# Kernel optimization log

Hardware: AMD Instinct MI355X
Metric: run time of the kernel (lower is better)

The kernel has to match this reference:

```python
import jax, jax.numpy as jnp
import numpy as np

B, Hm, Wm, Dm = 1, 32, 32, 32
N = Hm * Wm * Dm
C = 128
HEADS, DH = 8, 16
G = 32
L = 2
OUT = 1


def _ln(x, g, b):
    mu = jnp.mean(x, -1, keepdims=True)
    var = jnp.mean((x - mu) ** 2, -1, keepdims=True)
    return (x - mu) * jax.lax.rsqrt(var + 1e-5) * g + b


def setup_inputs() -> dict:
    key = jax.random.key(0)
    ks = iter(jax.random.split(key, 64))
    def nrm(shape, s=0.02):
        return jax.random.normal(next(ks), shape, jnp.float32) * s
    return {
        "x": jax.random.normal(next(ks), (B, N, 3), jnp.float32),
        "fx": jax.random.normal(next(ks), (B, N, 1), jnp.float32),
        "pre_w1": nrm((4, 2 * C)), "pre_b1": jnp.zeros((2 * C,), jnp.float32),
        "pre_w2": nrm((2 * C, C)), "pre_b2": jnp.zeros((C,), jnp.float32),
        "placeholder": jax.random.uniform(next(ks), (C,), jnp.float32) / C,
        "ln1_g": jnp.ones((L, C), jnp.float32), "ln1_b": jnp.zeros((L, C), jnp.float32),
        "convx_w": nrm((L, C, C, 3, 3, 3)), "convx_b": jnp.zeros((L, C), jnp.float32),
        "convfx_w": nrm((L, C, C, 3, 3, 3)), "convfx_b": jnp.zeros((L, C), jnp.float32),
        "slice_w": nrm((L, DH, G), 0.1), "slice_b": jnp.zeros((L, G), jnp.float32),
        "temperature": jnp.full((L, 1, HEADS, 1, 1), 0.5, jnp.float32),
        "wq": nrm((L, DH, DH), 0.1), "wk": nrm((L, DH, DH), 0.1), "wv": nrm((L, DH, DH), 0.1),
        "wo": nrm((L, HEADS * DH, C)), "bo": jnp.zeros((L, C), jnp.float32),
        "ln2_g": jnp.ones((L, C), jnp.float32), "ln2_b": jnp.zeros((L, C), jnp.float32),
        "mlp_w1": nrm((L, C, C)), "mlp_b1": jnp.zeros((L, C), jnp.float32),
        "mlp_w2": nrm((L, C, C)), "mlp_b2": jnp.zeros((L, C), jnp.float32),
        "ln3_g": jnp.ones((C,), jnp.float32), "ln3_b": jnp.zeros((C,), jnp.float32),
        "out_w": nrm((C, OUT)), "out_b": jnp.zeros((OUT,), jnp.float32),
    }


def _conv3d(x, w, b):
    # x: [B,C,H,W,D], w: [O,I,3,3,3], SAME padding (kernel//2) as torch Conv3d
    y = jax.lax.conv_general_dilated(x, w, (1, 1, 1), "SAME",
                                     dimension_numbers=("NCDHW", "OIDHW", "NCDHW"))
    return y + b[None, :, None, None, None]


def _physics_attn(z, cw_x, cb_x, cw_fx, cb_fx, sw, sb, temp, wq, wk, wv, wo, bo):
    # z: [B, N, C] -> structured mesh conv projections -> slice attention
    xg = z.reshape(B, Hm, Wm, Dm, C).transpose(0, 4, 1, 2, 3)  # [B,C,H,W,D]

    def split_heads(t):  # [B,I,H,W,D] -> [B,heads,N,dh]
        return t.transpose(0, 2, 3, 4, 1).reshape(B, N, HEADS, DH).transpose(0, 2, 1, 3)

    x_mid = split_heads(_conv3d(xg, cw_x, cb_x))
    fx_mid = split_heads(_conv3d(xg, cw_fx, cb_fx))
    # slice assignment weights: [B,heads,N,G], temperature-scaled softmax
    slice_logits = (x_mid @ sw + sb) / temp
    swt = jax.nn.softmax(slice_logits, axis=-1)
    norm = jnp.sum(swt, axis=2)  # [B,heads,G]
    tok = jnp.einsum("bhnc,bhng->bhgc", fx_mid, swt) / (norm + 1e-5)[..., None]
    q, k, v = tok @ wq, tok @ wk, tok @ wv  # [B,heads,G,dh]
    attn = jax.nn.softmax((q @ k.transpose(0, 1, 3, 2)) * (DH ** -0.5), axis=-1)
    ot = attn @ v  # [B,heads,G,dh]
    out = jnp.einsum("bhgc,bhng->bhnc", ot, swt)  # de-slice back to tokens
    out = out.transpose(0, 2, 1, 3).reshape(B, N, HEADS * DH)
    return out @ wo + bo


def reference(x, fx, pre_w1, pre_b1, pre_w2, pre_b2, placeholder,
              ln1_g, ln1_b, convx_w, convx_b, convfx_w, convfx_b,
              slice_w, slice_b, temperature, wq, wk, wv, wo, bo,
              ln2_g, ln2_b, mlp_w1, mlp_b1, mlp_w2, mlp_b2,
              ln3_g, ln3_b, out_w, out_b):
    h = jnp.concatenate([x, fx], axis=-1)  # [B,N,space+fun]
    z = jax.nn.gelu(h @ pre_w1 + pre_b1, approximate=False) @ pre_w2 + pre_b2 + placeholder
    for l in range(L):
        zn = _ln(z, ln1_g[l], ln1_b[l])
        z = _physics_attn(zn, convx_w[l], convx_b[l], convfx_w[l], convfx_b[l],
                          slice_w[l], slice_b[l], temperature[l],
                          wq[l], wk[l], wv[l], wo[l], bo[l]) + z
        zn = _ln(z, ln2_g[l], ln2_b[l])
        z = jax.nn.gelu(zn @ mlp_w1[l] + mlp_b1[l], approximate=False) @ mlp_w2[l] + mlp_b2[l] + z
    return _ln(z, ln3_g, ln3_b) @ out_w + out_b
```

## Files before the change

kernel.cpp:

```cpp
#include <hip/hip_runtime.h>
#include <hip/hip_bf16.h>

#define DEV __device__ __forceinline__

constexpr int N   = 32768;
constexpr int TOTAL_IN = 2038481;

constexpr int OFF_X        = 0;
constexpr int OFF_FX       = 98304;
constexpr int OFF_PRE_W1   = 131072;
constexpr int OFF_PRE_B1   = 132096;
constexpr int OFF_PRE_W2   = 132352;
constexpr int OFF_PRE_B2   = 165120;
constexpr int OFF_PLACE    = 165248;
constexpr int OFF_LN1_G    = 165376;
constexpr int OFF_LN1_B    = 165632;
constexpr int OFF_CONVX_W  = 165888;
constexpr int OFF_CONVX_B  = 1050624;
constexpr int OFF_CONVFX_W = 1050880;
constexpr int OFF_CONVFX_B = 1935616;
constexpr int OFF_SLICE_W  = 1935872;
constexpr int OFF_SLICE_B  = 1936896;
constexpr int OFF_TEMP     = 1936960;
constexpr int OFF_WQ       = 1936976;
constexpr int OFF_WK       = 1937488;
constexpr int OFF_WV       = 1938000;
constexpr int OFF_WO       = 1938512;
constexpr int OFF_BO       = 1971280;
constexpr int OFF_LN2_G    = 1971536;
constexpr int OFF_LN2_B    = 1971792;
constexpr int OFF_MLP_W1   = 1972048;
constexpr int OFF_MLP_B1   = 2004816;
constexpr int OFF_MLP_W2   = 2005072;
constexpr int OFF_MLP_B2   = 2037840;
constexpr int OFF_LN3_G    = 2038096;
constexpr int OFF_LN3_B    = 2038224;
constexpr int OFF_OUT_W    = 2038352;
constexpr int OFF_OUT_B    = 2038480;

__device__ __constant__ int d_PRE[32] = {
  0, 98304, 131072, 132096, 132352, 165120, 165248, 165376, 165632,
  165888, 1050624, 1050880, 1935616, 1935872, 1936896, 1936960, 1936976,
  1937488, 1938000, 1938512, 1971280, 1971536, 1971792, 1972048, 2004816,
  2005072, 2037840, 2038096, 2038224, 2038352, 2038480, 2038481
};

constexpr size_t F_IN   = 16;
constexpr size_t F_WT   = 2038512;
constexpr size_t F_Z    = F_WT   + 1769472;
constexpr size_t F_ZN   = F_Z    + 4194304;
constexpr size_t F_CONV = F_ZN   + 4194304;
constexpr size_t F_SWT  = F_CONV + 8388608;
constexpr size_t F_TOKP = F_SWT  + 8388608;
constexpr size_t F_TOK2 = F_TOKP + 1114112;
constexpr size_t F_OT   = F_TOK2 + 34816;
constexpr size_t F_WP   = F_OT   + 4096;
constexpr size_t F_END  = F_WP   + 65536;

struct InPtrs { const void* p[31]; };

typedef short short8v  __attribute__((ext_vector_type(8)));
typedef float float4v  __attribute__((ext_vector_type(4)));
#define MFMA16(A,B,C) __builtin_amdgcn_mfma_f32_16x16x32_bf16(A,B,C,0,0,0)

DEV float geluf(float x) { return 0.5f * x * (1.0f + erff(x * 0.70710678118654752f)); }
DEV short f2bs(float x) { union { __hip_bfloat16 h; short s; } c; c.h = __float2bfloat16(x); return c.s; }

__global__ void k_convert(InPtrs ptrs, float* __restrict__ ws) {
  const unsigned tw = *(const unsigned*)ptrs.p[15];
  const bool isbf = (tw == 0x3F003F00u);
  int stride = gridDim.x * blockDim.x;
  for (int e = blockIdx.x * blockDim.x + threadIdx.x; e < TOTAL_IN; e += stride) {
    int lo = 0, hi = 30;
#pragma unroll
    for (int it = 0; it < 5; ++it) {
      int mid = (lo + hi + 1) >> 1;
      if (e >= d_PRE[mid]) lo = mid; else hi = mid - 1;
    }
    int loc = e - d_PRE[lo];
    float v;
    if (isbf) {
      unsigned short u = ((const unsigned short*)ptrs.p[lo])[loc];
      unsigned uu = ((unsigned)u) << 16;
      v = __uint_as_float(uu);
    } else {
      v = ((const float*)ptrs.p[lo])[loc];
    }
    ws[F_IN + e] = v;
  }
}

__global__ void k_wtrans(const float* __restrict__ ip, short* __restrict__ wtf) {
  int f = blockIdx.x * 256 + threadIdx.x;
  if (f >= 221184) return;
  int lane = f & 63;
  int rest = f >> 6;
  int ntile = rest & 15;
  int r2 = rest >> 4;
  int layer = r2 / 108;
  int kt = r2 - layer * 108;
  int icb = kt / 27, tap = kt - icb * 27;
  int oc = ntile * 16 + (lane & 15);
  int ic0 = icb * 32 + (lane >> 4) * 8;
  const float* cw = ip + (oc < 128 ? OFF_CONVX_W : OFF_CONVFX_W);
  int o = oc & 127;
  const float* src = cw + ((size_t)(layer * 128 + o) * 128) * 27 + tap;
  short8v out;
#pragma unroll
  for (int j = 0; j < 8; ++j) out[j] = f2bs(src[(ic0 + j) * 27]);
  *(short8v*)(wtf + (size_t)f * 8) = out;
}

__global__ void k_wpack(const float* __restrict__ ip, short* __restrict__ wp) {
  int f = blockIdx.x * 256 + threadIdx.x;
  if (f >= 16384) return;
  int lane = f & 63;
  int t = f >> 6;
  int srcoff, kt, nt;
  if (t < 64) { srcoff = OFF_PRE_W2; kt = t >> 3; nt = t & 7; }
  else {
    int r = t - 64, l = r / 96, r2 = r - l * 96;
    int which = r2 >> 5, idx2 = r2 & 31;
    kt = idx2 >> 3; nt = idx2 & 7;
    srcoff = (which == 0 ? OFF_MLP_W1 : (which == 1 ? OFF_MLP_W2 : OFF_WO)) + l * 16384;
  }
  int k0 = kt * 32 + (lane >> 4) * 8;
  int n = nt * 16 + (lane & 15);
  const float* src = ip + srcoff + (size_t)k0 * 128 + n;
  short8v out;
#pragma unroll
  for (int j = 0; j < 8; ++j) out[j] = f2bs(src[(size_t)j * 128]);
  *(short8v*)(wp + (size_t)f * 8) = out;
}

__global__ __launch_bounds__(256)
void k_prenet(const float* __restrict__ ip, const short* __restrict__ wp,
              float* __restrict__ z, short* __restrict__ znb) {
  __shared__ float w1s[1024], b1s[256], cvec[128], g1s[128], be1s[128];
  __shared__ float xv[64][4];
  __shared__ __align__(16) short ts[64 * 264];
  int tid = threadIdx.x;
  int wv = tid >> 6, lane = tid & 63;
  int m = lane & 15, q = lane >> 4;
  int n0 = blockIdx.x * 64;
  for (int i = tid; i < 1024; i += 256) w1s[i] = ip[OFF_PRE_W1 + i];
  b1s[tid] = ip[OFF_PRE_B1 + tid];
  if (tid < 128) {
    cvec[tid] = ip[OFF_PRE_B2 + tid] + ip[OFF_PLACE + tid];
    g1s[tid]  = ip[OFF_LN1_G + tid];
    be1s[tid] = ip[OFF_LN1_B + tid];
  }
  if (tid < 64) {
    xv[tid][0] = ip[OFF_X + (n0 + tid) * 3 + 0];
    xv[tid][1] = ip[OFF_X + (n0 + tid) * 3 + 1];
    xv[tid][2] = ip[OFF_X + (n0 + tid) * 3 + 2];
    xv[tid][3] = ip[OFF_FX + n0 + tid];
  }
  __syncthreads();
  {
    float w0 = w1s[tid], wA = w1s[256 + tid], wB = w1s[512 + tid], wC = w1s[768 + tid];
    float bb = b1s[tid];
    for (int t = 0; t < 64; ++t) {
      float hv = bb + xv[t][0] * w0 + xv[t][1] * wA + xv[t][2] * wB + xv[t][3] * wC;
      ts[t * 264 + tid] = f2bs(geluf(hv));
    }
  }
  __syncthreads();
  const short8v* pwf = (const short8v*)wp;
  float4v acc[8];
#pragma unroll
  for (int nt = 0; nt < 8; ++nt) acc[nt] = (float4v){0.f, 0.f, 0.f, 0.f};
  for (int kt = 0; kt < 8; ++kt) {
    short8v A = *(const short8v*)(ts + (wv * 16 + m) * 264 + kt * 32 + q * 8);
#pragma unroll
    for (int nt = 0; nt < 8; ++nt)
      acc[nt] = MFMA16(A, pwf[(kt * 8 + nt) * 64 + lane], acc[nt]);
  }
  float vz[8][4];
#pragma unroll
  for (int nt = 0; nt < 8; ++nt) {
    int col = nt * 16 + m;
#pragma unroll
    for (int r = 0; r < 4; ++r) {
      vz[nt][r] = acc[nt][r] + cvec[col];
      z[(size_t)(n0 + wv * 16 + q * 4 + r) * 128 + col] = vz[nt][r];
    }
  }
#pragma unroll
  for (int r = 0; r < 4; ++r) {
    float s1 = 0.f, s2 = 0.f;
#pragma unroll
    for (int nt = 0; nt < 8; ++nt) { float v = vz[nt][r]; s1 += v; s2 += v * v; }
#pragma unroll
    for (int off = 1; off < 16; off <<= 1) { s1 += __shfl_xor(s1, off); s2 += __shfl_xor(s2, off); }
    float mu = s1 * (1.0f / 128.0f);
    float var = s2 * (1.0f / 128.0f) - mu * mu;
    float rst = 1.0f / sqrtf(var + 1e-5f);
    size_t rowb = (size_t)(n0 + wv * 16 + q * 4 + r) * 128;
#pragma unroll
    for (int nt = 0; nt < 8; ++nt) {
      int col = nt * 16 + m;
      znb[rowb + col] = f2bs((vz[nt][r] - mu) * rst * g1s[col] + be1s[col]);
    }
  }
}

__global__ __launch_bounds__(256)
void k_conv(const float* __restrict__ ip, const short* __restrict__ znb,
            const short* __restrict__ wtf, float* __restrict__ cv, int layer) {
  __shared__ __align__(16) short halo[13056];
  int tid = threadIdx.x;
  int wv = tid >> 6, lane = tid & 63;
  int m = lane & 15, q = lane >> 4;
  int n0 = blockIdx.x * 64;
  int h = n0 >> 10, w0 = (n0 >> 5) & 31;
  float bias_r[4];
#pragma unroll
  for (int nt = 0; nt < 4; ++nt) {
    int oc = (wv * 4 + nt) * 16 + m;
    bias_r[nt] = (oc < 128) ? ip[OFF_CONVX_B + layer * 128 + oc]
                            : ip[OFF_CONVFX_B + layer * 128 + (oc - 128)];
  }
  float4v acc[4][4];
#pragma unroll
  for (int a = 0; a < 4; ++a)
#pragma unroll
    for (int b = 0; b < 4; ++b) acc[a][b] = (float4v){0.f, 0.f, 0.f, 0.f};

  const short8v* wf = (const short8v*)wtf + (size_t)layer * 110592 + (wv * 4) * 64 + lane;
  short8v bc0 = wf[0], bc1 = wf[64], bc2 = wf[128], bc3 = wf[192];

  int tap = 0, icb = 0;
  for (int kt = 0; kt < 108; ++kt) {
    if (tap == 0) {
      __syncthreads();
      for (int pr = tid; pr < 408; pr += 256) {
        int line = pr / 34, dpos = pr - line * 34;
        int hh2 = h + (line >> 2) - 1, ww2 = w0 + (line & 3) - 1, dd2 = dpos - 1;
        bool ok = ((unsigned)hh2 < 32u) && ((unsigned)ww2 < 32u) && ((unsigned)dd2 < 32u);
        int tok = (hh2 << 10) + (ww2 << 5) + dd2;
#pragma unroll
        for (int qq = 0; qq < 4; ++qq) {
          short8v v = (short8v){0, 0, 0, 0, 0, 0, 0, 0};
          if (ok) v = *(const short8v*)(znb + (size_t)tok * 128 + icb * 32 + qq * 8);
          *(short8v*)(halo + qq * 3264 + pr * 8) = v;
        }
      }
      __syncthreads();
    }
    int ktn = (kt + 1 < 108) ? kt + 1 : kt;
    const short8v* wn = wf + (size_t)ktn * 1024;
    short8v bn0 = wn[0], bn1 = wn[64], bn2 = wn[128], bn3 = wn[192];

    int ta = tap / 9, rem = tap - ta * 9, tb = rem / 3, tc = rem - tb * 3;
    const short* hp = halo + q * 3264 + (((ta * 4 + tb) * 34) + tc + m) * 8;
    short8v A0 = *(const short8v*)(hp);
    short8v A1 = *(const short8v*)(hp + 128);
    short8v A2 = *(const short8v*)(hp + 272);
    short8v A3 = *(const short8v*)(hp + 400);

    acc[0][0] = MFMA16(A0, bc0, acc[0][0]);
    acc[1][0] = MFMA16(A1, bc0, acc[1][0]);
    acc[2][0] = MFMA16(A2, bc0, acc[2][0]);
    acc[3][0] = MFMA16(A3, bc0, acc[3][0]);
    acc[0][1] = MFMA16(A0, bc1, acc[0][1]);
    acc[1][1] = MFMA16(A1, bc1, acc[1][1]);
    acc[2][1] = MFMA16(A2, bc1, acc[2][1]);
    acc[3][1] = MFMA16(A3, bc1, acc[3][1]);
    acc[0][2] = MFMA16(A0, bc2, acc[0][2]);
    acc[1][2] = MFMA16(A1, bc2, acc[1][2]);
    acc[2][2] = MFMA16(A2, bc2, acc[2][2]);
    acc[3][2] = MFMA16(A3, bc2, acc[3][2]);
    acc[0][3] = MFMA16(A0, bc3, acc[0][3]);
    acc[1][3] = MFMA16(A1, bc3, acc[1][3]);
    acc[2][3] = MFMA16(A2, bc3, acc[2][3]);
    acc[3][3] = MFMA16(A3, bc3, acc[3][3]);

    bc0 = bn0; bc1 = bn1; bc2 = bn2; bc3 = bn3;
    if (++tap == 27) { tap = 0; ++icb; }
  }
#pragma unroll
  for (int mt = 0; mt < 4; ++mt) {
    float* cp = cv + (size_t)(n0 + mt * 16 + q * 4) * 256 + (wv * 4) * 16 + m;
#pragma unroll
    for (int nt = 0; nt < 4; ++nt) {
#pragma unroll
      for (int r = 0; r < 4; ++r)
        cp[(size_t)r * 256 + nt * 16] = acc[mt][nt][r] + bias_r[nt];
    }
  }
}

__global__ __launch_bounds__(256)
void k_slice(const float* __restrict__ ip, const float* __restrict__ cv,
             short* __restrict__ swtb, float* __restrict__ tokp, int layer) {
  __shared__ float sws[512], sbs[32], its[8];
  __shared__ float swl[32 * 257];
  __shared__ float fxl[32 * 128];
  int tid = threadIdx.x;
  for (int i = tid; i < 512; i += 256) sws[i] = ip[OFF_SLICE_W + layer * 512 + i];
  if (tid < 32) sbs[tid] = ip[OFF_SLICE_B + layer * 32 + tid];
  if (tid < 8)  its[tid] = 1.0f / ip[OFF_TEMP + layer * 8 + tid];
  float4 ta0 = make_float4(0,0,0,0), ta1 = ta0, ta2 = ta0, ta3 = ta0;
  float np = 0.f;
  for (int s = 0; s < 4; ++s) {
    int tbase = blockIdx.x * 128 + s * 32;
    __syncthreads();
    for (int i = tid; i < 1024; i += 256) {
      int t = i >> 5, c4 = (i & 31) * 4;
      *(float4*)&fxl[t * 128 + c4] = *(const float4*)&cv[(size_t)(tbase + t) * 256 + 128 + c4];
    }
    {
      int t = tid >> 3, hh = tid & 7;
      float xm[16];
#pragma unroll
      for (int qq = 0; qq < 4; ++qq)
        *(float4*)&xm[qq * 4] = *(const float4*)&cv[(size_t)(tbase + t) * 256 + hh * 16 + qq * 4];
      float lg[32];
      float itv = its[hh];
#pragma unroll
      for (int g = 0; g < 32; ++g) {
        float sacc = sbs[g];
#pragma unroll
        for (int j = 0; j < 16; ++j) sacc += xm[j] * sws[j * 32 + g];
        lg[g] = sacc * itv;
      }
      float mx = -1e30f;
#pragma unroll
      for (int g = 0; g < 32; ++g) mx = fmaxf(mx, lg[g]);
      float sum = 0.f;
#pragma unroll
      for (int g = 0; g < 32; ++g) { lg[g] = expf(lg[g] - mx); sum += lg[g]; }
      float inv = 1.0f / sum;
#pragma unroll
      for (int g = 0; g < 32; ++g) {
        lg[g] *= inv;
        swl[t * 257 + hh * 32 + g] = lg[g];
      }
#pragma unroll
      for (int qq = 0; qq < 4; ++qq) {
        short8v pk;
#pragma unroll
        for (int j = 0; j < 8; ++j) pk[j] = f2bs(lg[qq * 8 + j]);
        *(short8v*)(swtb + (size_t)(tbase + t) * 256 + hh * 32 + qq * 8) = pk;
      }
    }
    __syncthreads();
    {
      int ah = tid >> 5, ag = tid & 31;
      for (int t2 = 0; t2 < 32; ++t2) {
        float sv = swl[t2 * 257 + ah * 32 + ag];
        np += sv;
        const float* f = &fxl[t2 * 128 + ah * 16];
        float4 f0 = *(const float4*)&f[0], f1 = *(const float4*)&f[4];
        float4 f2 = *(const float4*)&f[8], f3 = *(const float4*)&f[12];
        ta0.x += sv * f0.x; ta0.y += sv * f0.y; ta0.z += sv * f0.z; ta0.w += sv * f0.w;
        ta1.x += sv * f1.x; ta1.y += sv * f1.y; ta1.z += sv * f1.z; ta1.w += sv * f1.w;
        ta2.x += sv * f2.x; ta2.y += sv * f2.y; ta2.z += sv * f2.z; ta2.w += sv * f2.w;
        ta3.x += sv * f3.x; ta3.y += sv * f3.y; ta3.z += sv * f3.z; ta3.w += sv * f3.w;
      }
    }
  }
  int ah = tid >> 5, ag = tid & 31;
  size_t base = (size_t)blockIdx.x * 4352 + (size_t)(ah * 32 + ag) * 16;
  *(float4*)&tokp[base + 0]  = ta0;
  *(float4*)&tokp[base + 4]  = ta1;
  *(float4*)&tokp[base + 8]  = ta2;
  *(float4*)&tokp[base + 12] = ta3;
  tokp[(size_t)blockIdx.x * 4352 + 4096 + ah * 32 + ag] = np;
}

__global__ void k_tokred1(const float* __restrict__ tokp, float* __restrict__ tok2) {
  int ogrp = blockIdx.x % 17, bgrp = blockIdx.x / 17;
  int o = ogrp * 256 + threadIdx.x;
  float s = 0.f;
  int b0 = bgrp * 32;
#pragma unroll 8
  for (int b = b0; b < b0 + 32; ++b) s += tokp[(size_t)b * 4352 + o];
  tok2[(size_t)bgrp * 4352 + o] = s;
}

__global__ __launch_bounds__(256)
void k_attn(const float* __restrict__ ip, const float* __restrict__ tok2,
            float* __restrict__ ot, int layer) {
  __shared__ float trs[4352];
  __shared__ float kk[256 * 17], vv[256 * 17];
  int tid = threadIdx.x;
  for (int i = tid; i < 4352; i += 256) {
    float s = 0.f;
#pragma unroll
    for (int b = 0; b < 8; ++b) s += tok2[(size_t)b * 4352 + i];
    trs[i] = s;
  }
  __syncthreads();
  int hh = tid >> 5;
  const float* wq = ip + OFF_WQ + layer * 256;
  const float* wk = ip + OFF_WK + layer * 256;
  const float* wv = ip + OFF_WV + layer * 256;
  float inv = 1.0f / (trs[4096 + tid] + 1e-5f);
  float t[16];
#pragma unroll
  for (int c = 0; c < 16; ++c) t[c] = trs[tid * 16 + c] * inv;
  float q[16];
#pragma unroll
  for (int c = 0; c < 16; ++c) {
    float aq = 0.f, ak = 0.f, av = 0.f;
#pragma unroll
    for (int j = 0; j < 16; ++j) {
      float tv = t[j];
      aq += tv * wq[j * 16 + c];
      ak += tv * wk[j * 16 + c];
      av += tv * wv[j * 16 + c];
    }
    q[c] = aq;
    kk[tid * 17 + c] = ak;
    vv[tid * 17 + c] = av;
  }
  __syncthreads();
  float sc[32];
  float mx = -1e30f;
#pragma unroll
  for (int g2 = 0; g2 < 32; ++g2) {
    float s = 0.f;
#pragma unroll
    for (int c = 0; c < 16; ++c) s += q[c] * kk[(hh * 32 + g2) * 17 + c];
    s *= 0.25f;
    sc[g2] = s; mx = fmaxf(mx, s);
  }
  float sum = 0.f;
#pragma unroll
  for (int g2 = 0; g2 < 32; ++g2) { sc[g2] = expf(sc[g2] - mx); sum += sc[g2]; }
  float inv2 = 1.0f / sum;
  float o[16];
#pragma unroll
  for (int c = 0; c < 16; ++c) o[c] = 0.f;
#pragma unroll
  for (int g2 = 0; g2 < 32; ++g2) {
    float p = sc[g2] * inv2;
#pragma unroll
    for (int c = 0; c < 16; ++c) o[c] += p * vv[(hh * 32 + g2) * 17 + c];
  }
#pragma unroll
  for (int c = 0; c < 16; ++c) ot[tid * 16 + c] = o[c];
}

__global__ __launch_bounds__(256)
void k_fused(const float* __restrict__ ip, const short* __restrict__ swtb,
             const float* __restrict__ ot, const short* __restrict__ wp,
             float* __restrict__ z, short* __restrict__ znb,
             void* __restrict__ dout, const void* __restrict__ tempraw, int layer) {
  __shared__ __align__(16) short otb[4096];
  __shared__ __align__(16) short al[8704];
  __shared__ __align__(16) short znt[8704];
  __shared__ float bol[128], b1s[128], b2s[128], g2s[128], be2s[128], lng[128], lnb[128], ows[128];
  int tid = threadIdx.x;
  int wv = tid >> 6, lane = tid & 63;
  int m = lane & 15, q = lane >> 4;
  int n0 = blockIdx.x * 64;
  if (tid < 128) {
    bol[tid]  = ip[OFF_BO + layer * 128 + tid];
    b1s[tid]  = ip[OFF_MLP_B1 + layer * 128 + tid];
    b2s[tid]  = ip[OFF_MLP_B2 + layer * 128 + tid];
    g2s[tid]  = ip[OFF_LN2_G + layer * 128 + tid];
    be2s[tid] = ip[OFF_LN2_B + layer * 128 + tid];
    if (layer == 0) {
      lng[tid] = ip[OFF_LN1_G + 128 + tid];
      lnb[tid] = ip[OFF_LN1_B + 128 + tid];
      ows[tid] = 0.f;
    } else {
      lng[tid] = ip[OFF_LN3_G + tid];
      lnb[tid] = ip[OFF_LN3_B + tid];
      ows[tid] = ip[OFF_OUT_W + tid];
    }
  }
  for (int i = tid; i < 4096; i += 256) {
    int h = i >> 9, r = i & 511, ln = r >> 3, j = r & 7;
    int g = (ln >> 4) * 8 + j, dh = ln & 15;
    otb[i] = f2bs(ot[h * 512 + g * 16 + dh]);
  }
  __syncthreads();
  float4v accd[8];
#pragma unroll
  for (int h = 0; h < 8; ++h) accd[h] = (float4v){0.f, 0.f, 0.f, 0.f};
#pragma unroll
  for (int h = 0; h < 8; ++h) {
    short8v A = *(const short8v*)(swtb + (size_t)(n0 + wv * 16 + m) * 256 + h * 32 + q * 8);
    accd[h] = MFMA16(A, *(const short8v*)(otb + h * 512 + lane * 8), accd[h]);
  }
#pragma unroll
  for (int h = 0; h < 8; ++h)
#pragma unroll
    for (int r = 0; r < 4; ++r)
      al[(wv * 16 + q * 4 + r) * 136 + h * 16 + m] = f2bs(accd[h][r]);
  __syncthreads();
  const short8v* wof = (const short8v*)(wp + (size_t)(128 + 96 * layer) * 512);
  float4v a2[8];
#pragma unroll
  for (int nt = 0; nt < 8; ++nt) a2[nt] = (float4v){0.f, 0.f, 0.f, 0.f};
  for (int kt = 0; kt < 4; ++kt) {
    short8v A = *(const short8v*)(al + (wv * 16 + m) * 136 + kt * 32 + q * 8);
#pragma unroll
    for (int nt = 0; nt < 8; ++nt)
      a2[nt] = MFMA16(A, wof[(kt * 8 + nt) * 64 + lane], a2[nt]);
  }
  float vmid[8][4];
#pragma unroll
  for (int nt = 0; nt < 8; ++nt) {
    int col = nt * 16 + m;
#pragma unroll
    for (int r = 0; r < 4; ++r)
      vmid[nt][r] = z[(size_t)(n0 + wv * 16 + q * 4 + r) * 128 + col] + a2[nt][r] + bol[col];
  }
#pragma unroll
  for (int r = 0; r < 4; ++r) {
    float s1 = 0.f, s2 = 0.f;
#pragma unroll
    for (int nt = 0; nt < 8; ++nt) { float v = vmid[nt][r]; s1 += v; s2 += v * v; }
#pragma unroll
    for (int off = 1; off < 16; off <<= 1) { s1 += __shfl_xor(s1, off); s2 += __shfl_xor(s2, off); }
    float mu = s1 * (1.0f / 128.0f);
    float var = s2 * (1.0f / 128.0f) - mu * mu;
    float rst = 1.0f / sqrtf(var + 1e-5f);
#pragma unroll
    for (int nt = 0; nt < 8; ++nt) {
      int col = nt * 16 + m;
      znt[(wv * 16 + q * 4 + r) * 136 + col] = f2bs((vmid[nt][r] - mu) * rst * g2s[col] + be2s[col]);
    }
  }
  __syncthreads();
  const short8v* w1f = (const short8v*)(wp + (size_t)(64 + 96 * layer) * 512);
  const short8v* w2f = (const short8v*)(wp + (size_t)(96 + 96 * layer) * 512);
  float4v acc[8];
#pragma unroll
  for (int nt = 0; nt < 8; ++nt) acc[nt] = (float4v){0.f, 0.f, 0.f, 0.f};
  for (int kt = 0; kt < 4; ++kt) {
    short8v A = *(const short8v*)(znt + (wv * 16 + m) * 136 + kt * 32 + q * 8);
#pragma unroll
    for (int nt = 0; nt < 8; ++nt)
      acc[nt] = MFMA16(A, w1f[(kt * 8 + nt) * 64 + lane], acc[nt]);
  }
  __syncthreads();
#pragma unroll
  for (int nt = 0; nt < 8; ++nt) {
    int col = nt * 16 + m;
#pragma unroll
    for (int r = 0; r < 4; ++r)
      al[(wv * 16 + q * 4 + r) * 136 + col] = f2bs(geluf(acc[nt][r] + b1s[col]));
  }
  __syncthreads();
  float4v a4[8];
#pragma unroll
  for (int nt = 0; nt < 8; ++nt) a4[nt] = (float4v){0.f, 0.f, 0.f, 0.f};
  for (int kt = 0; kt < 4; ++kt) {
    short8v A = *(const short8v*)(al + (wv * 16 + m) * 136 + kt * 32 + q * 8);
#pragma unroll
    for (int nt = 0; nt < 8; ++nt)
      a4[nt] = MFMA16(A, w2f[(kt * 8 + nt) * 64 + lane], a4[nt]);
  }
  float vfin[8][4];
#pragma unroll
  for (int nt = 0; nt < 8; ++nt) {
    int col = nt * 16 + m;
#pragma unroll
    for (int r = 0; r < 4; ++r) {
      vfin[nt][r] = vmid[nt][r] + a4[nt][r] + b2s[col];
      z[(size_t)(n0 + wv * 16 + q * 4 + r) * 128 + col] = vfin[nt][r];
    }
  }
#pragma unroll
  for (int r = 0; r < 4; ++r) {
    float s1 = 0.f, s2 = 0.f;
#pragma unroll
    for (int nt = 0; nt < 8; ++nt) { float v = vfin[nt][r]; s1 += v; s2 += v * v; }
#pragma unroll
    for (int off = 1; off < 16; off <<= 1) { s1 += __shfl_xor(s1, off); s2 += __shfl_xor(s2, off); }
    float mu = s1 * (1.0f / 128.0f);
    float var = s2 * (1.0f / 128.0f) - mu * mu;
    float rst = 1.0f / sqrtf(var + 1e-5f);
    int n = n0 + wv * 16 + q * 4 + r;
    if (layer == 0) {
      size_t rowb = (size_t)n * 128;
#pragma unroll
      for (int nt = 0; nt < 8; ++nt) {
        int col = nt * 16 + m;
        znb[rowb + col] = f2bs((vfin[nt][r] - mu) * rst * lng[col] + lnb[col]);
      }
    } else {
      float contrib = 0.f;
#pragma unroll
      for (int nt = 0; nt < 8; ++nt) {
        int col = nt * 16 + m;
        contrib += ((vfin[nt][r] - mu) * rst * lng[col] + lnb[col]) * ows[col];
      }
#pragma unroll
      for (int off = 1; off < 16; off <<= 1) contrib += __shfl_xor(contrib, off);
      if (m == 0) {
        float res = contrib + ip[OFF_OUT_B];
        unsigned tw = *(const unsigned*)tempraw;
        if (tw == 0x3F003F00u) ((__hip_bfloat16*)dout)[n] = __float2bfloat16(res);
        else                   ((float*)dout)[n] = res;
      }
    }
  }
}

extern "C" void kernel_launch(void* const* d_in, const int* in_sizes, int n_in,
                              void* d_out, int out_size, void* d_ws, size_t ws_size,
                              hipStream_t stream) {
  (void)in_sizes; (void)out_size; (void)ws_size;
  if (n_in < 31) return;
  float* ws   = (float*)d_ws;
  float* ip   = ws + F_IN;
  short* wtf  = (short*)(ws + F_WT);
  float* z    = ws + F_Z;
  short* znb  = (short*)(ws + F_ZN);
  float* cv   = ws + F_CONV;
  short* swtb = (short*)(ws + F_SWT);
  float* tkp  = ws + F_TOKP;
  float* tk2  = ws + F_TOK2;
  float* ot   = ws + F_OT;
  short* wp   = (short*)(ws + F_WP);

  InPtrs P;
  for (int i = 0; i < 31; ++i) P.p[i] = d_in[i];

  k_convert<<<2048, 256, 0, stream>>>(P, ws);
  k_wtrans <<<864, 256, 0, stream>>>(ip, wtf);
  k_wpack  <<<64, 256, 0, stream>>>(ip, wp);
  k_prenet <<<512, 256, 0, stream>>>(ip, wp, z, znb);
  for (int l = 0; l < 2; ++l) {
    k_conv   <<<512, 256, 0, stream>>>(ip, znb, wtf, cv, l);
    k_slice  <<<256, 256, 0, stream>>>(ip, cv, swtb, tkp, l);
    k_tokred1<<<136, 256, 0, stream>>>(tkp, tk2);
    k_attn   <<<1, 256, 0, stream>>>(ip, tk2, ot, l);
    k_fused  <<<512, 256, 0, stream>>>(ip, swtb, ot, wp, z, znb, d_out, d_in[15], l);
  }
}
```

Measured before the change: 474.3 us.

## Fuse attention into fused kernel, enlarge conv tiles, read conv weights directly

Several changes land together. k_convert now skips the conv weight ranges, and k_wtrans reads the raw inputs directly (bf16 or fp32), which removes a large fp32 staging copy. k_conv now uses 512-thread blocks covering 128 tokens with a bigger shared halo, and it prefetches the next tap's A fragments so LDS reads overlap the MFMAs. The single-block k_attn launch is folded into k_fused, so every block redundantly recomputes the tiny slice attention. That removes one launch and one round trip through global memory, but adds redundant compute and larger shared memory in each fused block.

```diff
diff --git a/kernel.cpp b/kernel.cpp
--- a/kernel.cpp
+++ b/kernel.cpp
@@ -71,6 +71,7 @@
   const bool isbf = (tw == 0x3F003F00u);
   int stride = gridDim.x * blockDim.x;
   for (int e = blockIdx.x * blockDim.x + threadIdx.x; e < TOTAL_IN; e += stride) {
+    if ((e >= OFF_CONVX_W && e < OFF_CONVX_B) || (e >= OFF_CONVFX_W && e < OFF_CONVFX_B)) continue;
     int lo = 0, hi = 30;
 #pragma unroll
     for (int it = 0; it < 5; ++it) {
@@ -90,7 +91,9 @@
   }
 }
 
-__global__ void k_wtrans(const float* __restrict__ ip, short* __restrict__ wtf) {
+__global__ void k_wtrans(const void* __restrict__ cwxr, const void* __restrict__ cwfr,
+                         const void* __restrict__ tempraw, short* __restrict__ wtf) {
+  const bool isbf = (*(const unsigned*)tempraw == 0x3F003F00u);
   int f = blockIdx.x * 256 + threadIdx.x;
   if (f >= 221184) return;
   int lane = f & 63;
@@ -102,12 +105,19 @@
   int icb = kt / 27, tap = kt - icb * 27;
   int oc = ntile * 16 + (lane & 15);
   int ic0 = icb * 32 + (lane >> 4) * 8;
-  const float* cw = ip + (oc < 128 ? OFF_CONVX_W : OFF_CONVFX_W);
+  const void* cw = (oc < 128) ? cwxr : cwfr;
   int o = oc & 127;
-  const float* src = cw + ((size_t)(layer * 128 + o) * 128) * 27 + tap;
+  size_t base = ((size_t)(layer * 128 + o) * 128) * 27 + tap;
   short8v out;
-#pragma unroll
-  for (int j = 0; j < 8; ++j) out[j] = f2bs(src[(ic0 + j) * 27]);
+  if (isbf) {
+    const unsigned short* src = (const unsigned short*)cw + base;
+#pragma unroll
+    for (int j = 0; j < 8; ++j) out[j] = (short)src[(size_t)(ic0 + j) * 27];
+  } else {
+    const float* src = (const float*)cw + base;
+#pragma unroll
+    for (int j = 0; j < 8; ++j) out[j] = f2bs(src[(size_t)(ic0 + j) * 27]);
+  }
   *(short8v*)(wtf + (size_t)f * 8) = out;
 }
 
@@ -205,19 +215,20 @@
   }
 }
 
-__global__ __launch_bounds__(256)
+__global__ __launch_bounds__(512, 2)
 void k_conv(const float* __restrict__ ip, const short* __restrict__ znb,
             const short* __restrict__ wtf, float* __restrict__ cv, int layer) {
-  __shared__ __align__(16) short halo[13056];
+  __shared__ __align__(16) short halo[19584];
   int tid = threadIdx.x;
   int wv = tid >> 6, lane = tid & 63;
   int m = lane & 15, q = lane >> 4;
-  int n0 = blockIdx.x * 64;
+  int half = wv >> 2, ocq = wv & 3;
+  int n0 = blockIdx.x * 128;
   int h = n0 >> 10, w0 = (n0 >> 5) & 31;
   float bias_r[4];
 #pragma unroll
   for (int nt = 0; nt < 4; ++nt) {
-    int oc = (wv * 4 + nt) * 16 + m;
+    int oc = (ocq * 4 + nt) * 16 + m;
     bias_r[nt] = (oc < 128) ? ip[OFF_CONVX_B + layer * 128 + oc]
                             : ip[OFF_CONVFX_B + layer * 128 + (oc - 128)];
   }
@@ -227,61 +238,74 @@
 #pragma unroll
     for (int b = 0; b < 4; ++b) acc[a][b] = (float4v){0.f, 0.f, 0.f, 0.f};
 
-  const short8v* wf = (const short8v*)wtf + (size_t)layer * 110592 + (wv * 4) * 64 + lane;
+  const short8v* wf = (const short8v*)wtf + (size_t)layer * 110592 + (ocq * 4) * 64 + lane;
+  const short* hq = halo + q * 4896;
+  const int rowA = half * 2;
   short8v bc0 = wf[0], bc1 = wf[64], bc2 = wf[128], bc3 = wf[192];
-
-  int tap = 0, icb = 0;
-  for (int kt = 0; kt < 108; ++kt) {
-    if (tap == 0) {
-      __syncthreads();
-      for (int pr = tid; pr < 408; pr += 256) {
-        int line = pr / 34, dpos = pr - line * 34;
-        int hh2 = h + (line >> 2) - 1, ww2 = w0 + (line & 3) - 1, dd2 = dpos - 1;
-        bool ok = ((unsigned)hh2 < 32u) && ((unsigned)ww2 < 32u) && ((unsigned)dd2 < 32u);
-        int tok = (hh2 << 10) + (ww2 << 5) + dd2;
-#pragma unroll
-        for (int qq = 0; qq < 4; ++qq) {
-          short8v v = (short8v){0, 0, 0, 0, 0, 0, 0, 0};
-          if (ok) v = *(const short8v*)(znb + (size_t)tok * 128 + icb * 32 + qq * 8);
-          *(short8v*)(halo + qq * 3264 + pr * 8) = v;
-        }
-      }
-      __syncthreads();
-    }
-    int ktn = (kt + 1 < 108) ? kt + 1 : kt;
-    const short8v* wn = wf + (size_t)ktn * 1024;
-    short8v bn0 = wn[0], bn1 = wn[64], bn2 = wn[128], bn3 = wn[192];
-
-    int ta = tap / 9, rem = tap - ta * 9, tb = rem / 3, tc = rem - tb * 3;
-    const short* hp = halo + q * 3264 + (((ta * 4 + tb) * 34) + tc + m) * 8;
-    short8v A0 = *(const short8v*)(hp);
-    short8v A1 = *(const short8v*)(hp + 128);
-    short8v A2 = *(const short8v*)(hp + 272);
-    short8v A3 = *(const short8v*)(hp + 400);
-
-    acc[0][0] = MFMA16(A0, bc0, acc[0][0]);
-    acc[1][0] = MFMA16(A1, bc0, acc[1][0]);
-    acc[2][0] = MFMA16(A2, bc0, acc[2][0]);
-    acc[3][0] = MFMA16(A3, bc0, acc[3][0]);
-    acc[0][1] = MFMA16(A0, bc1, acc[0][1]);
-    acc[1][1] = MFMA16(A1, bc1, acc[1][1]);
-    acc[2][1] = MFMA16(A2, bc1, acc[2][1]);
-    acc[3][1] = MFMA16(A3, bc1, acc[3][1]);
-    acc[0][2] = MFMA16(A0, bc2, acc[0][2]);
-    acc[1][2] = MFMA16(A1, bc2, acc[1][2]);
-    acc[2][2] = MFMA16(A2, bc2, acc[2][2]);
-    acc[3][2] = MFMA16(A3, bc2, acc[3][2]);
-    acc[0][3] = MFMA16(A0, bc3, acc[0][3]);
-    acc[1][3] = MFMA16(A1, bc3, acc[1][3]);
-    acc[2][3] = MFMA16(A2, bc3, acc[2][3]);
-    acc[3][3] = MFMA16(A3, bc3, acc[3][3]);
-
-    bc0 = bn0; bc1 = bn1; bc2 = bn2; bc3 = bn3;
-    if (++tap == 27) { tap = 0; ++icb; }
+  short8v A0, A1, A2, A3;
+
+  for (int icb = 0; icb < 4; ++icb) {
+    __syncthreads();
+    for (int pr = tid; pr < 612; pr += 512) {
+      int line = pr / 34, dpos = pr - line * 34;
+      int lh = line / 6, lw = line - lh * 6;
+      int hh2 = h + lh - 1, ww2 = w0 + lw - 1, dd2 = dpos - 1;
+      bool ok = ((unsigned)hh2 < 32u) && ((unsigned)ww2 < 32u) && ((unsigned)dd2 < 32u);
+      int tok = (hh2 << 10) + (ww2 << 5) + dd2;
+#pragma unroll
+      for (int qq = 0; qq < 4; ++qq) {
+        short8v v = (short8v){0, 0, 0, 0, 0, 0, 0, 0};
+        if (ok) v = *(const short8v*)(znb + (size_t)tok * 128 + icb * 32 + qq * 8);
+        *(short8v*)(halo + qq * 4896 + pr * 8) = v;
+      }
+    }
+    __syncthreads();
+    {
+      const short* hp = hq + (rowA * 34 + m) * 8;
+      A0 = *(const short8v*)(hp);
+      A1 = *(const short8v*)(hp + 128);
+      A2 = *(const short8v*)(hp + 272);
+      A3 = *(const short8v*)(hp + 400);
+    }
+    int ktb = icb * 27;
+    for (int tap = 0; tap < 27; ++tap) {
+      int kt = ktb + tap;
+      int ktn = (kt + 1 < 108) ? kt + 1 : kt;
+      const short8v* wn = wf + (size_t)ktn * 1024;
+      short8v bn0 = wn[0], bn1 = wn[64], bn2 = wn[128], bn3 = wn[192];
+      short8v An0, An1, An2, An3;
+      if (tap < 26) {
+        int tp = tap + 1;
+        int ta = tp / 9, rem = tp - ta * 9, tb = rem / 3, tc = rem - tb * 3;
+        const short* hp = hq + (((ta * 6 + rowA + tb) * 34) + tc + m) * 8;
+        An0 = *(const short8v*)(hp);
+        An1 = *(const short8v*)(hp + 128);
+        An2 = *(const short8v*)(hp + 272);
+        An3 = *(const short8v*)(hp + 400);
+      }
+      acc[0][0] = MFMA16(A0, bc0, acc[0][0]);
+      acc[1][0] = MFMA16(A1, bc0, acc[1][0]);
+      acc[2][0] = MFMA16(A2, bc0, acc[2][0]);
+      acc[3][0] = MFMA16(A3, bc0, acc[3][0]);
+      acc[0][1] = MFMA16(A0, bc1, acc[0][1]);
+      acc[1][1] = MFMA16(A1, bc1, acc[1][1]);
+      acc[2][1] = MFMA16(A2, bc1, acc[2][1]);
+      acc[3][1] = MFMA16(A3, bc1, acc[3][1]);
+      acc[0][2] = MFMA16(A0, bc2, acc[0][2]);
+      acc[1][2] = MFMA16(A1, bc2, acc[1][2]);
+      acc[2][2] = MFMA16(A2, bc2, acc[2][2]);
+      acc[3][2] = MFMA16(A3, bc2, acc[3][2]);
+      acc[0][3] = MFMA16(A0, bc3, acc[0][3]);
+      acc[1][3] = MFMA16(A1, bc3, acc[1][3]);
+      acc[2][3] = MFMA16(A2, bc3, acc[2][3]);
+      acc[3][3] = MFMA16(A3, bc3, acc[3][3]);
+      bc0 = bn0; bc1 = bn1; bc2 = bn2; bc3 = bn3;
+      if (tap < 26) { A0 = An0; A1 = An1; A2 = An2; A3 = An3; }
+    }
   }
 #pragma unroll
   for (int mt = 0; mt < 4; ++mt) {
-    float* cp = cv + (size_t)(n0 + mt * 16 + q * 4) * 256 + (wv * 4) * 16 + m;
+    float* cp = cv + (size_t)(n0 + half * 64 + mt * 16 + q * 4) * 256 + (ocq * 4) * 16 + m;
 #pragma unroll
     for (int nt = 0; nt < 4; ++nt) {
 #pragma unroll
@@ -381,78 +405,20 @@
 }
 
 __global__ __launch_bounds__(256)
-void k_attn(const float* __restrict__ ip, const float* __restrict__ tok2,
-            float* __restrict__ ot, int layer) {
-  __shared__ float trs[4352];
-  __shared__ float kk[256 * 17], vv[256 * 17];
-  int tid = threadIdx.x;
-  for (int i = tid; i < 4352; i += 256) {
-    float s = 0.f;
-#pragma unroll
-    for (int b = 0; b < 8; ++b) s += tok2[(size_t)b * 4352 + i];
-    trs[i] = s;
-  }
-  __syncthreads();
-  int hh = tid >> 5;
-  const float* wq = ip + OFF_WQ + layer * 256;
-  const float* wk = ip + OFF_WK + layer * 256;
-  const float* wv = ip + OFF_WV + layer * 256;
-  float inv = 1.0f / (trs[4096 + tid] + 1e-5f);
-  float t[16];
-#pragma unroll
-  for (int c = 0; c < 16; ++c) t[c] = trs[tid * 16 + c] * inv;
-  float q[16];
-#pragma unroll
-  for (int c = 0; c < 16; ++c) {
-    float aq = 0.f, ak = 0.f, av = 0.f;
-#pragma unroll
-    for (int j = 0; j < 16; ++j) {
-      float tv = t[j];
-      aq += tv * wq[j * 16 + c];
-      ak += tv * wk[j * 16 + c];
-      av += tv * wv[j * 16 + c];
-    }
-    q[c] = aq;
-    kk[tid * 17 + c] = ak;
-    vv[tid * 17 + c] = av;
-  }
-  __syncthreads();
-  float sc[32];
-  float mx = -1e30f;
-#pragma unroll
-  for (int g2 = 0; g2 < 32; ++g2) {
-    float s = 0.f;
-#pragma unroll
-    for (int c = 0; c < 16; ++c) s += q[c] * kk[(hh * 32 + g2) * 17 + c];
-    s *= 0.25f;
-    sc[g2] = s; mx = fmaxf(mx, s);
-  }
-  float sum = 0.f;
-#pragma unroll
-  for (int g2 = 0; g2 < 32; ++g2) { sc[g2] = expf(sc[g2] - mx); sum += sc[g2]; }
-  float inv2 = 1.0f / sum;
-  float o[16];
-#pragma unroll
-  for (int c = 0; c < 16; ++c) o[c] = 0.f;
-#pragma unroll
-  for (int g2 = 0; g2 < 32; ++g2) {
-    float p = sc[g2] * inv2;
-#pragma unroll
-    for (int c = 0; c < 16; ++c) o[c] += p * vv[(hh * 32 + g2) * 17 + c];
-  }
-#pragma unroll
-  for (int c = 0; c < 16; ++c) ot[tid * 16 + c] = o[c];
-}
-
-__global__ __launch_bounds__(256)
 void k_fused(const float* __restrict__ ip, const short* __restrict__ swtb,
-             const float* __restrict__ ot, const short* __restrict__ wp,
+             const float* __restrict__ tok2, const short* __restrict__ wp,
              float* __restrict__ z, short* __restrict__ znb,
              void* __restrict__ dout, const void* __restrict__ tempraw, int layer) {
-  __shared__ __align__(16) short otb[4096];
-  __shared__ __align__(16) short al[8704];
-  __shared__ __align__(16) short znt[8704];
-  __shared__ float bol[128], b1s[128], b2s[128], g2s[128], be2s[128], lng[128], lnb[128], ows[128];
+  __shared__ __align__(16) char smem[64512];
+  short* otb = (short*)smem;
+  float* bia = (float*)(smem + 8192);
+  float* trs = (float*)(smem + 12288);
+  short* znt = (short*)(smem + 12288);
+  float* kk  = (float*)(smem + 29696);
+  short* al  = (short*)(smem + 29696);
+  float* vvs = (float*)(smem + 47104);
+  float* bol = bia, *b1s = bia + 128, *b2s = bia + 256, *g2s = bia + 384;
+  float* be2s = bia + 512, *lng = bia + 640, *lnb = bia + 768, *ows = bia + 896;
   int tid = threadIdx.x;
   int wv = tid >> 6, lane = tid & 63;
   int m = lane & 15, q = lane >> 4;
@@ -473,10 +439,66 @@
       ows[tid] = ip[OFF_OUT_W + tid];
     }
   }
-  for (int i = tid; i < 4096; i += 256) {
-    int h = i >> 9, r = i & 511, ln = r >> 3, j = r & 7;
-    int g = (ln >> 4) * 8 + j, dh = ln & 15;
-    otb[i] = f2bs(ot[h * 512 + g * 16 + dh]);
+  for (int i = tid; i < 4352; i += 256) {
+    float s = 0.f;
+#pragma unroll
+    for (int b = 0; b < 8; ++b) s += tok2[(size_t)b * 4352 + i];
+    trs[i] = s;
+  }
+  __syncthreads();
+  float qv[16];
+  {
+    const float* wqp = ip + OFF_WQ + layer * 256;
+    const float* wkp = ip + OFF_WK + layer * 256;
+    const float* wvp = ip + OFF_WV + layer * 256;
+    float inv = 1.0f / (trs[4096 + tid] + 1e-5f);
+    float t[16];
+#pragma unroll
+    for (int c = 0; c < 16; ++c) t[c] = trs[tid * 16 + c] * inv;
+#pragma unroll
+    for (int c = 0; c < 16; ++c) {
+      float aq = 0.f, ak = 0.f, av = 0.f;
+#pragma unroll
+      for (int j = 0; j < 16; ++j) {
+        float tv = t[j];
+        aq += tv * wqp[j * 16 + c];
+        ak += tv * wkp[j * 16 + c];
+        av += tv * wvp[j * 16 + c];
+      }
+      qv[c] = aq;
+      kk[tid * 17 + c] = ak;
+      vvs[tid * 17 + c] = av;
+    }
+  }
+  __syncthreads();
+  {
+    int hh = tid >> 5, g = tid & 31;
+    float sc[32];
+    float mx = -1e30f;
+#pragma unroll
+    for (int g2 = 0; g2 < 32; ++g2) {
+      float s = 0.f;
+#pragma unroll
+      for (int c = 0; c < 16; ++c) s += qv[c] * kk[(hh * 32 + g2) * 17 + c];
+      s *= 0.25f;
+      sc[g2] = s; mx = fmaxf(mx, s);
+    }
+    float sum = 0.f;
+#pragma unroll
+    for (int g2 = 0; g2 < 32; ++g2) { sc[g2] = expf(sc[g2] - mx); sum += sc[g2]; }
+    float inv2 = 1.0f / sum;
+    float o[16];
+#pragma unroll
+    for (int c = 0; c < 16; ++c) o[c] = 0.f;
+#pragma unroll
+    for (int g2 = 0; g2 < 32; ++g2) {
+      float p = sc[g2] * inv2;
+#pragma unroll
+      for (int c = 0; c < 16; ++c) o[c] += p * vvs[(hh * 32 + g2) * 17 + c];
+    }
+#pragma unroll
+    for (int dh = 0; dh < 16; ++dh)
+      otb[hh * 512 + (((g >> 3) * 16 + dh) << 3) + (g & 7)] = f2bs(o[dh]);
   }
   __syncthreads();
   float4v accd[8];
@@ -487,6 +509,7 @@
     short8v A = *(const short8v*)(swtb + (size_t)(n0 + wv * 16 + m) * 256 + h * 32 + q * 8);
     accd[h] = MFMA16(A, *(const short8v*)(otb + h * 512 + lane * 8), accd[h]);
   }
+  __syncthreads();
 #pragma unroll
   for (int h = 0; h < 8; ++h)
 #pragma unroll
@@ -618,21 +641,19 @@
   short* swtb = (short*)(ws + F_SWT);
   float* tkp  = ws + F_TOKP;
   float* tk2  = ws + F_TOK2;
-  float* ot   = ws + F_OT;
   short* wp   = (short*)(ws + F_WP);
 
   InPtrs P;
   for (int i = 0; i < 31; ++i) P.p[i] = d_in[i];
 
-  k_convert<<<2048, 256, 0, stream>>>(P, ws);
-  k_wtrans <<<864, 256, 0, stream>>>(ip, wtf);
+  k_convert<<<512, 256, 0, stream>>>(P, ws);
+  k_wtrans <<<864, 256, 0, stream>>>(d_in[9], d_in[11], d_in[15], wtf);
   k_wpack  <<<64, 256, 0, stream>>>(ip, wp);
   k_prenet <<<512, 256, 0, stream>>>(ip, wp, z, znb);
   for (int l = 0; l < 2; ++l) {
-    k_conv   <<<512, 256, 0, stream>>>(ip, znb, wtf, cv, l);
+    k_conv   <<<256, 512, 0, stream>>>(ip, znb, wtf, cv, l);
     k_slice  <<<256, 256, 0, stream>>>(ip, cv, swtb, tkp, l);
     k_tokred1<<<136, 256, 0, stream>>>(tkp, tk2);
-    k_attn   <<<1, 256, 0, stream>>>(ip, tk2, ot, l);
-    k_fused  <<<512, 256, 0, stream>>>(ip, swtb, ot, wp, z, znb, d_out, d_in[15], l);
-  }
-}
+    k_fused  <<<512, 256, 0, stream>>>(ip, swtb, tk2, wp, z, znb, d_out, d_in[15], l);
+  }
+}
```

Measured after the change: 487.8 us. 1.03x slower.
